# Kernel optimization log

Hardware: AMD Instinct MI355X
Metric: run time of the kernel (lower is better)

The kernel has to match this reference:

```python
import jax, jax.numpy as jnp
import numpy as np

D_MODEL = 768
N_HEADS = 12
D_HEAD = D_MODEL // N_HEADS

def setup_inputs() -> dict:
    key = jax.random.key(0)
    ks = jax.random.split(key, 5)
    B, T = 2, 4096
    x = jax.random.normal(ks[0], (B, T, D_MODEL), dtype=jnp.float32)
    s_in = 1.0 / np.sqrt(D_MODEL)
    W_qkv = jax.random.normal(ks[1], (D_MODEL, 3 * D_MODEL), dtype=jnp.float32) * s_in
    b_qkv = jnp.zeros((3 * D_MODEL,), dtype=jnp.float32)
    W_proj = jax.random.normal(ks[2], (D_MODEL, D_MODEL), dtype=jnp.float32) * s_in
    b_proj = jnp.zeros((D_MODEL,), dtype=jnp.float32)
    return {"x": x, "W_qkv": W_qkv, "b_qkv": b_qkv, "W_proj": W_proj, "b_proj": b_proj}

def reference(x, W_qkv, b_qkv, W_proj, b_proj):
    B, T, C = x.shape
    qkv = x @ W_qkv + b_qkv                      # [B,T,3C]
    q, k, v = jnp.split(qkv, 3, axis=-1)
    def heads(t):
        return t.reshape(B, T, N_HEADS, D_HEAD).transpose(0, 2, 1, 3)  # [B,H,T,d]
    q, k, v = heads(q), heads(k), heads(v)
    scale = 1.0 / np.sqrt(D_HEAD)
    att = jnp.einsum('bhqd,bhkd->bhqk', q, k) * scale  # [B,H,T,T]
    causal = jnp.tril(jnp.ones((T, T), dtype=bool))
    att = jnp.where(causal[None, None], att, -jnp.inf)
    att = jax.nn.softmax(att, axis=-1)
    y = jnp.einsum('bhqk,bhkd->bhqd', att, v)          # [B,H,T,d]
    y = y.transpose(0, 2, 1, 3).reshape(B, T, C)
    return y @ W_proj + b_proj
```

## Files before the change

### kernel.cpp

```cpp
#include <hip/hip_runtime.h>
#include <hip/hip_bf16.h>

typedef __bf16 bf16_t;
typedef bf16_t bf16x4 __attribute__((ext_vector_type(4)));
typedef bf16_t bf16x8 __attribute__((ext_vector_type(8)));
typedef float  f32x4  __attribute__((ext_vector_type(4)));

#define TSEQ   4096
#define NBATCH 2
#define DMODEL 768
#define NHEADS 12
#define DHEAD  64
#define NTOK   (NBATCH*TSEQ)
#define NQKV   (3*DMODEL)

#define QSCALE 0.18033688011112042f
#define SMAX 24.0f

__device__ __forceinline__ f32x4 mfma16(bf16x8 a, bf16x8 b, f32x4 c) {
  return __builtin_amdgcn_mfma_f32_16x16x32_bf16(a, b, c, 0, 0, 0);
}

__device__ __forceinline__ void glds16(const bf16_t* g, bf16_t* l) {
  __builtin_amdgcn_global_load_lds(
      (const __attribute__((address_space(1))) void*)g,
      (__attribute__((address_space(3))) void*)l, 16, 0, 0);
}
__device__ __forceinline__ void glds16f(const float* g, float* l) {
  __builtin_amdgcn_global_load_lds(
      (const __attribute__((address_space(1))) void*)g,
      (__attribute__((address_space(3))) void*)l, 16, 0, 0);
}

__global__ __launch_bounds__(256) void k_transpose_cvt2(
    const float* __restrict__ W1, bf16_t* __restrict__ O1,
    const float* __restrict__ W2, bf16_t* __restrict__ O2) {
  __shared__ bf16_t tile[64][66];
  int t = blockIdx.x;
  const float* in; bf16_t* out; int R, C, c0, r0;
  if (t < 432) { in = W1; out = O1; R = DMODEL; C = NQKV;
                 c0 = (t % 36) * 64; r0 = (t / 36) * 64; }
  else { t -= 432; in = W2; out = O2; R = DMODEL; C = DMODEL;
         c0 = (t % 12) * 64; r0 = (t / 12) * 64; }
  const int tid = threadIdx.x;
  const int r = tid >> 2, cb = (tid & 3) * 16;
  const float* ip = in + (long)(r0 + r) * C + c0 + cb;
#pragma unroll
  for (int k = 0; k < 16; k += 4) {
    float4 v = *(const float4*)(ip + k);
    tile[r][cb + k + 0] = (bf16_t)v.x;
    tile[r][cb + k + 1] = (bf16_t)v.y;
    tile[r][cb + k + 2] = (bf16_t)v.z;
    tile[r][cb + k + 3] = (bf16_t)v.w;
  }
  __syncthreads();
  const int c = tid >> 2, rb = (tid & 3) * 16;
  bf16_t* op = out + (long)(c0 + c) * R + r0 + rb;
  bf16x8 v0, v1;
#pragma unroll
  for (int i = 0; i < 8; ++i) { v0[i] = tile[rb + i][c]; v1[i] = tile[rb + 8 + i][c]; }
  *(bf16x8*)(op) = v0;
  *(bf16x8*)(op + 8) = v1;
}

__global__ __launch_bounds__(256) void k_gemm_qkv(
    const float* __restrict__ X, const bf16_t* __restrict__ Bt,
    const float* __restrict__ bias,
    bf16_t* __restrict__ Qo, bf16_t* __restrict__ Ko, bf16_t* __restrict__ Vt) {
  __shared__ __align__(16) float  Asf[2 * 128 * 32];
  __shared__ __align__(16) bf16_t Bs[2 * 128 * 32];
  const int wave = threadIdx.x >> 6;
  const int lane = threadIdx.x & 63;
  const int quad = lane >> 4;
  const int l16  = lane & 15;
  const int m0 = blockIdx.x * 128;
  const int n0 = blockIdx.y * 128;

  const int arow = lane >> 3;
  const int achk = (lane & 7) ^ arow;
  const float* x0 = X + (long)(m0 + wave * 8 + arow) * DMODEL + achk * 4;
  const int srow = lane >> 2;
  const int scol = (lane & 3) * 8;
  const bf16_t* b0 = Bt + (long)(n0 + wave * 16 + srow) * DMODEL + scol;

  f32x4 acc[2][8] = {};

#pragma unroll
  for (int i = 0; i < 4; ++i)
    glds16f(x0 + (long)i * 32 * DMODEL, Asf + (i * 32 + wave * 8) * 32);
  glds16(b0,               Bs + wave * 16 * 32);
  glds16(b0 + 64 * DMODEL, Bs + (64 + wave * 16) * 32);
  __syncthreads();

  const int sk = l16 & 7;
  for (int ks = 0; ks < DMODEL / 32; ++ks) {
    const int p = ks & 1;
    if (ks + 1 < DMODEL / 32) {
      const int k1 = (ks + 1) * 32;
      float*  Asx = (p ? Asf : Asf + 128 * 32);
      bf16_t* Bsx = (p ? Bs : Bs + 128 * 32);
#pragma unroll
      for (int i = 0; i < 4; ++i)
        glds16f(x0 + (long)i * 32 * DMODEL + k1, Asx + (i * 32 + wave * 8) * 32);
      glds16(b0 + k1,               Bsx + wave * 16 * 32);
      glds16(b0 + 64 * DMODEL + k1, Bsx + (64 + wave * 16) * 32);
    }
    const float*  Ap = Asf + p * (128 * 32);
    const bf16_t* Bp = Bs + p * (128 * 32);

    const int r0 = wave * 32 + l16, r1 = r0 + 16;
    f32x4 a0lo = *(const f32x4*)(Ap + r0 * 32 + (((2 * quad)     ^ sk) << 2));
    f32x4 a0hi = *(const f32x4*)(Ap + r0 * 32 + (((2 * quad + 1) ^ sk) << 2));
    f32x4 a1lo = *(const f32x4*)(Ap + r1 * 32 + (((2 * quad)     ^ sk) << 2));
    f32x4 a1hi = *(const f32x4*)(Ap + r1 * 32 + (((2 * quad + 1) ^ sk) << 2));
    bf16x8 af0, af1;
#pragma unroll
    for (int j = 0; j < 4; ++j) {
      af0[j] = (bf16_t)a0lo[j]; af0[4 + j] = (bf16_t)a0hi[j];
      af1[j] = (bf16_t)a1lo[j]; af1[4 + j] = (bf16_t)a1hi[j];
    }
#pragma unroll
    for (int nt = 0; nt < 8; ++nt) {
      bf16x8 bfm = *(const bf16x8*)(Bp + (nt * 16 + l16) * 32 + quad * 8);
      acc[0][nt] = mfma16(af0, bfm, acc[0][nt]);
      acc[1][nt] = mfma16(af1, bfm, acc[1][nt]);
    }
    __syncthreads();
  }

#pragma unroll
  for (int s = 0; s < 2; ++s)
#pragma unroll
    for (int nt = 0; nt < 8; ++nt) {
      const int n = n0 + nt * 16 + l16;
      const float bv = bias[n];
      const int mb = m0 + wave * 32 + s * 16 + quad * 4;
      const int b = mb >> 12;
      const int t = mb & 4095;
      if (n < DMODEL) {
        const int h = n >> 6, d = n & 63;
        bf16_t* qp = Qo + (((long)(b * NHEADS + h) * TSEQ + t) << 6) + d;
#pragma unroll
        for (int j = 0; j < 4; ++j)
          qp[(long)j << 6] = (bf16_t)((acc[s][nt][j] + bv) * QSCALE);
      } else if (n < 2 * DMODEL) {
        const int n2 = n - DMODEL, h = n2 >> 6, d = n2 & 63;
        bf16_t* kp = Ko + (((long)(b * NHEADS + h) * TSEQ + t) << 6) + d;
#pragma unroll
        for (int j = 0; j < 4; ++j)
          kp[(long)j << 6] = (bf16_t)(acc[s][nt][j] + bv);
      } else {
        const int n2 = n - 2 * DMODEL, h = n2 >> 6, d = n2 & 63;
        bf16x4 v;
#pragma unroll
        for (int j = 0; j < 4; ++j) v[j] = (bf16_t)(acc[s][nt][j] + bv);
        *(bf16x4*)(Vt + ((long)(b * NHEADS + h) * DHEAD + d) * TSEQ + t) = v;
      }
    }
}

__global__ __launch_bounds__(256) void k_gemm_proj(
    const bf16_t* __restrict__ P0, const bf16_t* __restrict__ P1,
    const float* __restrict__ L0, const float* __restrict__ L1,
    const bf16_t* __restrict__ Bt, const float* __restrict__ bias,
    float* __restrict__ out) {
  __shared__ __align__(16) bf16_t A0s[2 * 64 * 32];
  __shared__ __align__(16) bf16_t A1s[2 * 64 * 32];
  __shared__ __align__(16) bf16_t Bs[2 * 128 * 32];
  __shared__ float linv[NHEADS * 64];
  const int wave = threadIdx.x >> 6;
  const int lane = threadIdx.x & 63;
  const int quad = lane >> 4;
  const int l16  = lane & 15;
  const int m0 = blockIdx.x * 64;
  const int n0 = blockIdx.y * 128;
  const int b  = m0 >> 12;
  const int t0 = m0 & 4095;

  for (int i = threadIdx.x; i < NHEADS * 64; i += 256) {
    const int h = i >> 6, t = i & 63;
    const long idx = (long)(b * NHEADS + h) * TSEQ + t0 + t;
    linv[i] = 1.f / (L0[idx] + L1[idx]);
  }

  const int srow = lane >> 2;
  const int scol = (lane & 3) * 8;
  const bf16_t* b0 = Bt + (long)(n0 + wave * 16 + srow) * DMODEL + scol;
  const long arowbase = (long)(t0 + wave * 16 + srow);

  f32x4 acc[8] = {};

  {
    const long off = (((long)(b * NHEADS + 0) * TSEQ + arowbase) << 6) + scol;
    glds16(P0 + off, A0s + wave * 16 * 32);
    glds16(P1 + off, A1s + wave * 16 * 32);
  }
  glds16(b0,               Bs + wave * 16 * 32);
  glds16(b0 + 64 * DMODEL, Bs + (64 + wave * 16) * 32);
  __syncthreads();

  for (int ks = 0; ks < DMODEL / 32; ++ks) {
    const int p = ks & 1;
    if (ks + 1 < DMODEL / 32) {
      const int k1 = (ks + 1) * 32;
      const int ksn = ks + 1;
      bf16_t* A0x = (p ? A0s : A0s + 64 * 32);
      bf16_t* A1x = (p ? A1s : A1s + 64 * 32);
      bf16_t* Bsx = (p ? Bs : Bs + 128 * 32);
      const long off = (((long)(b * NHEADS + (ksn >> 1)) * TSEQ + arowbase) << 6)
                       + ((ksn & 1) << 5) + scol;
      glds16(P0 + off, A0x + wave * 16 * 32);
      glds16(P1 + off, A1x + wave * 16 * 32);
      glds16(b0 + k1,               Bsx + wave * 16 * 32);
      glds16(b0 + 64 * DMODEL + k1, Bsx + (64 + wave * 16) * 32);
    }
    const bf16_t* A0p = A0s + p * (64 * 32);
    const bf16_t* A1p = A1s + p * (64 * 32);
    const bf16_t* Bp  = Bs + p * (128 * 32);

    bf16x8 a0 = *(const bf16x8*)(A0p + (wave * 16 + l16) * 32 + quad * 8);
    bf16x8 a1 = *(const bf16x8*)(A1p + (wave * 16 + l16) * 32 + quad * 8);
    const float li = linv[(ks >> 1) * 64 + wave * 16 + l16];
    bf16x8 af;
#pragma unroll
    for (int j = 0; j < 8; ++j)
      af[j] = (bf16_t)(((float)a0[j] + (float)a1[j]) * li);
#pragma unroll
    for (int nt = 0; nt < 8; ++nt) {
      bf16x8 bfm = *(const bf16x8*)(Bp + (nt * 16 + l16) * 32 + quad * 8);
      acc[nt] = mfma16(af, bfm, acc[nt]);
    }
    __syncthreads();
  }

#pragma unroll
  for (int nt = 0; nt < 8; ++nt) {
    const int n = n0 + nt * 16 + l16;
    const float bv = bias[n];
#pragma unroll
    for (int j = 0; j < 4; ++j) {
      const int m = m0 + wave * 16 + quad * 4 + j;
      out[(long)m * DMODEL + n] = acc[nt][j] + bv;
    }
  }
}

__global__ __launch_bounds__(256, 2) void k_attn(
    const bf16_t* __restrict__ Q, const bf16_t* __restrict__ K,
    const bf16_t* __restrict__ Vt,
    bf16_t* __restrict__ P0, bf16_t* __restrict__ P1,
    float* __restrict__ L0, float* __restrict__ L1) {
  __shared__ __align__(16) bf16_t kbuf[2][64 * 64];
  __shared__ __align__(16) bf16_t vbuf[2][64 * 64];
  const int wave = threadIdx.x >> 6;
  const int lane = threadIdx.x & 63;
  const int quad = lane >> 4;
  const int l16  = lane & 15;
  const int bh = blockIdx.x;
  const int qt = 15 - (blockIdx.y >> 1);
  const int sp = blockIdx.y & 1;
  const int half = 2 * qt + 2;
  const int c0 = sp ? half : 0;
  const int niter = half;
  bf16_t* Pp = sp ? P1 : P0;
  float*  Lp = sp ? L1 : L0;

  const bf16_t* Qh = Q + ((long)bh * TSEQ << 6);
  const bf16_t* Kh = K + ((long)bh * TSEQ << 6);
  const bf16_t* Vh = Vt + (long)bh * DHEAD * TSEQ;

  const int qbase = qt * 256 + wave * 64;

  bf16x8 qf[4][2];
#pragma unroll
  for (int s = 0; s < 4; ++s) {
    const bf16_t* qrow = Qh + ((long)(qbase + s * 16 + l16) << 6);
    qf[s][0] = *(const bf16x8*)(qrow + quad * 8);
    qf[s][1] = *(const bf16x8*)(qrow + 32 + quad * 8);
  }

  f32x4 acc[4][4] = {};
  float lS[4] = {0.f, 0.f, 0.f, 0.f};
  const f32x4 minit = {-SMAX, -SMAX, -SMAX, -SMAX};

  const int kperm = ((l16 >> 2) << 3) + (l16 & 3);
  const int swl = l16 & 7;
  const int srow = lane >> 3;
  const int cV = (lane & 7) ^ (srow & 7);
  const int cK0 = (lane & 7) ^ (srow & 3);
  const int cK1 = cK0 ^ 4;
  const int r0a = wave * 16, r0b = wave * 16 + 8;

  {
    const int k00 = c0 << 6;
    glds16(Kh + ((long)(k00 + r0a + srow) << 6) + cK0 * 8, &kbuf[0][r0a * 64]);
    glds16(Kh + ((long)(k00 + r0b + srow) << 6) + cK1 * 8, &kbuf[0][r0b * 64]);
    glds16(Vh + (long)(r0a + srow) * TSEQ + k00 + cV * 8,  &vbuf[0][r0a * 64]);
    glds16(Vh + (long)(r0b + srow) * TSEQ + k00 + cV * 8,  &vbuf[0][r0b * 64]);
  }
  __syncthreads();

  for (int ci = 0; ci < niter; ++ci) {
    const int p = ci & 1;
    const int k0 = (c0 + ci) << 6;
    if (ci + 1 < niter) {
      const int k1 = k0 + 64;
      glds16(Kh + ((long)(k1 + r0a + srow) << 6) + cK0 * 8, &kbuf[1 - p][r0a * 64]);
      glds16(Kh + ((long)(k1 + r0b + srow) << 6) + cK1 * 8, &kbuf[1 - p][r0b * 64]);
      glds16(Vh + (long)(r0a + srow) * TSEQ + k1 + cV * 8,  &vbuf[1 - p][r0a * 64]);
      glds16(Vh + (long)(r0b + srow) * TSEQ + k1 + cV * 8,  &vbuf[1 - p][r0b * 64]);
    }
    const bf16_t* kb = kbuf[p];
    const bf16_t* vb = vbuf[p];

#pragma unroll
    for (int g = 0; g < 2; ++g) {
      const int rw0 = (g * 32 + kperm) * 64;
      const int rw1 = (g * 32 + 4 + kperm) * 64;
      bf16x8 kf00 = *(const bf16x8*)(kb + rw0 + ((quad ^ swl) << 3));
      bf16x8 kf01 = *(const bf16x8*)(kb + rw0 + (((quad + 4) ^ swl) << 3));
      bf16x8 kf10 = *(const bf16x8*)(kb + rw1 + ((quad ^ swl) << 3));
      bf16x8 kf11 = *(const bf16x8*)(kb + rw1 + (((quad + 4) ^ swl) << 3));
      const bool domask = (k0 + g * 32 + 31 > qbase);

      bf16x8 pf[4];
#pragma unroll
      for (int s = 0; s < 4; ++s) {
        f32x4 st0 = minit, st1 = minit;
        st0 = mfma16(kf00, qf[s][0], st0);
        st0 = mfma16(kf01, qf[s][1], st0);
        st1 = mfma16(kf10, qf[s][0], st1);
        st1 = mfma16(kf11, qf[s][1], st1);
        if (domask) {
          const int qS = qbase + s * 16 + l16;
          const int kb0 = k0 + g * 32 + quad * 8;
#pragma unroll
          for (int j = 0; j < 4; ++j) {
            if (kb0 + j > qS)     st0[j] = -1e30f;
            if (kb0 + 4 + j > qS) st1[j] = -1e30f;
          }
        }
        float rs = 0.f;
#pragma unroll
        for (int j = 0; j < 4; ++j) {
          float e0 = __builtin_amdgcn_exp2f(st0[j]);
          float e1 = __builtin_amdgcn_exp2f(st1[j]);
          rs += e0 + e1;
          pf[s][j]     = (bf16_t)e0;
          pf[s][4 + j] = (bf16_t)e1;
        }
        lS[s] += rs;
      }
#pragma unroll
      for (int dt = 0; dt < 4; ++dt) {
        const int row = dt * 16 + l16;
        bf16x8 vf = *(const bf16x8*)(vb + row * 64 + ((((g << 2) + quad) ^ swl) << 3));
#pragma unroll
        for (int s = 0; s < 4; ++s)
          acc[s][dt] = mfma16(vf, pf[s], acc[s][dt]);
      }
    }
    __syncthreads();
  }

#pragma unroll
  for (int s = 0; s < 4; ++s) {
    lS[s] += __shfl_xor(lS[s], 16);
    lS[s] += __shfl_xor(lS[s], 32);
  }
#pragma unroll
  for (int s = 0; s < 4; ++s) {
    const int qS = qbase + s * 16 + l16;
    bf16_t* prow = Pp + (((long)bh * TSEQ + qS) << 6);
#pragma unroll
    for (int dt = 0; dt < 4; ++dt) {
      bf16x4 w;
#pragma unroll
      for (int j = 0; j < 4; ++j) w[j] = (bf16_t)acc[s][dt][j];
      *(bf16x4*)(prow + dt * 16 + quad * 4) = w;
    }
    if (quad == 0) Lp[(long)bh * TSEQ + qS] = lS[s];
  }
}

extern "C" void kernel_launch(void* const* d_in, const int* in_sizes, int n_in,
                              void* d_out, int out_size, void* d_ws, size_t ws_size,
                              hipStream_t stream) {
  (void)in_sizes; (void)n_in; (void)out_size; (void)ws_size;
  const float* x     = (const float*)d_in[0];
  const float* Wqkv  = (const float*)d_in[1];
  const float* bqkv  = (const float*)d_in[2];
  const float* Wproj = (const float*)d_in[3];
  const float* bproj = (const float*)d_in[4];
  float* out = (float*)d_out;

  char* ws = (char*)d_ws;
  bf16_t* wqkv_t  = (bf16_t*)ws; ws += (long)NQKV * DMODEL * 2;
  bf16_t* wproj_t = (bf16_t*)ws; ws += (long)DMODEL * DMODEL * 2;
  bf16_t* Qb      = (bf16_t*)ws; ws += (long)NTOK * DMODEL * 2;
  bf16_t* Kb      = (bf16_t*)ws; ws += (long)NTOK * DMODEL * 2;
  bf16_t* Vtb     = (bf16_t*)ws; ws += (long)NTOK * DMODEL * 2;
  bf16_t* P0b     = (bf16_t*)ws; ws += (long)NTOK * DMODEL * 2;
  bf16_t* P1b     = (bf16_t*)ws; ws += (long)NTOK * DMODEL * 2;
  float*  L0b     = (float*)ws;  ws += (long)NHEADS * NBATCH * TSEQ * 4;
  float*  L1b     = (float*)ws;  ws += (long)NHEADS * NBATCH * TSEQ * 4;

  k_transpose_cvt2<<<576, 256, 0, stream>>>(Wqkv, wqkv_t, Wproj, wproj_t);
  k_gemm_qkv<<<dim3(NTOK / 128, NQKV / 128), 256, 0, stream>>>(x, wqkv_t, bqkv, Qb, Kb, Vtb);
  k_attn<<<dim3(NBATCH * NHEADS, 32), 256, 0, stream>>>(Qb, Kb, Vtb, P0b, P1b, L0b, L1b);
  k_gemm_proj<<<dim3(NTOK / 64, DMODEL / 128), 256, 0, stream>>>(
      P0b, P1b, L0b, L1b, wproj_t, bproj, out);
}
```

Before: 224.5 us.

## Split attention KV range four ways instead of two

The attention kernel now splits each query tile's causal key range into four chunks instead of two. This doubles the grid to 64 blocks per head-batch. Each chunk writes its own unnormalized partial output and row sum, and the projection GEMM sums all four before normalizing. The aim is more parallelism and better load balance across CUs, at the cost of extra partial-buffer traffic and more loads in the projection GEMM.

```diff
diff --git a/kernel.cpp b/kernel.cpp
--- a/kernel.cpp
+++ b/kernel.cpp
@@ -161,11 +161,15 @@
 
 __global__ __launch_bounds__(256) void k_gemm_proj(
     const bf16_t* __restrict__ P0, const bf16_t* __restrict__ P1,
+    const bf16_t* __restrict__ P2, const bf16_t* __restrict__ P3,
     const float* __restrict__ L0, const float* __restrict__ L1,
+    const float* __restrict__ L2, const float* __restrict__ L3,
     const bf16_t* __restrict__ Bt, const float* __restrict__ bias,
     float* __restrict__ out) {
   __shared__ __align__(16) bf16_t A0s[2 * 64 * 32];
   __shared__ __align__(16) bf16_t A1s[2 * 64 * 32];
+  __shared__ __align__(16) bf16_t A2s[2 * 64 * 32];
+  __shared__ __align__(16) bf16_t A3s[2 * 64 * 32];
   __shared__ __align__(16) bf16_t Bs[2 * 128 * 32];
   __shared__ float linv[NHEADS * 64];
   const int wave = threadIdx.x >> 6;
@@ -180,7 +184,7 @@
   for (int i = threadIdx.x; i < NHEADS * 64; i += 256) {
     const int h = i >> 6, t = i & 63;
     const long idx = (long)(b * NHEADS + h) * TSEQ + t0 + t;
-    linv[i] = 1.f / (L0[idx] + L1[idx]);
+    linv[i] = 1.f / (L0[idx] + L1[idx] + L2[idx] + L3[idx]);
   }
 
   const int srow = lane >> 2;
@@ -194,6 +198,8 @@
     const long off = (((long)(b * NHEADS + 0) * TSEQ + arowbase) << 6) + scol;
     glds16(P0 + off, A0s + wave * 16 * 32);
     glds16(P1 + off, A1s + wave * 16 * 32);
+    glds16(P2 + off, A2s + wave * 16 * 32);
+    glds16(P3 + off, A3s + wave * 16 * 32);
   }
   glds16(b0,               Bs + wave * 16 * 32);
   glds16(b0 + 64 * DMODEL, Bs + (64 + wave * 16) * 32);
@@ -206,25 +212,34 @@
       const int ksn = ks + 1;
       bf16_t* A0x = (p ? A0s : A0s + 64 * 32);
       bf16_t* A1x = (p ? A1s : A1s + 64 * 32);
+      bf16_t* A2x = (p ? A2s : A2s + 64 * 32);
+      bf16_t* A3x = (p ? A3s : A3s + 64 * 32);
       bf16_t* Bsx = (p ? Bs : Bs + 128 * 32);
       const long off = (((long)(b * NHEADS + (ksn >> 1)) * TSEQ + arowbase) << 6)
                        + ((ksn & 1) << 5) + scol;
       glds16(P0 + off, A0x + wave * 16 * 32);
       glds16(P1 + off, A1x + wave * 16 * 32);
+      glds16(P2 + off, A2x + wave * 16 * 32);
+      glds16(P3 + off, A3x + wave * 16 * 32);
       glds16(b0 + k1,               Bsx + wave * 16 * 32);
       glds16(b0 + 64 * DMODEL + k1, Bsx + (64 + wave * 16) * 32);
     }
     const bf16_t* A0p = A0s + p * (64 * 32);
     const bf16_t* A1p = A1s + p * (64 * 32);
+    const bf16_t* A2p = A2s + p * (64 * 32);
+    const bf16_t* A3p = A3s + p * (64 * 32);
     const bf16_t* Bp  = Bs + p * (128 * 32);
 
     bf16x8 a0 = *(const bf16x8*)(A0p + (wave * 16 + l16) * 32 + quad * 8);
     bf16x8 a1 = *(const bf16x8*)(A1p + (wave * 16 + l16) * 32 + quad * 8);
+    bf16x8 a2 = *(const bf16x8*)(A2p + (wave * 16 + l16) * 32 + quad * 8);
+    bf16x8 a3 = *(const bf16x8*)(A3p + (wave * 16 + l16) * 32 + quad * 8);
     const float li = linv[(ks >> 1) * 64 + wave * 16 + l16];
     bf16x8 af;
 #pragma unroll
     for (int j = 0; j < 8; ++j)
-      af[j] = (bf16_t)(((float)a0[j] + (float)a1[j]) * li);
+      af[j] = (bf16_t)((((float)a0[j] + (float)a1[j]) +
+                        ((float)a2[j] + (float)a3[j])) * li);
 #pragma unroll
     for (int nt = 0; nt < 8; ++nt) {
       bf16x8 bfm = *(const bf16x8*)(Bp + (nt * 16 + l16) * 32 + quad * 8);
@@ -249,7 +264,9 @@
     const bf16_t* __restrict__ Q, const bf16_t* __restrict__ K,
     const bf16_t* __restrict__ Vt,
     bf16_t* __restrict__ P0, bf16_t* __restrict__ P1,
-    float* __restrict__ L0, float* __restrict__ L1) {
+    bf16_t* __restrict__ P2, bf16_t* __restrict__ P3,
+    float* __restrict__ L0, float* __restrict__ L1,
+    float* __restrict__ L2, float* __restrict__ L3) {
   __shared__ __align__(16) bf16_t kbuf[2][64 * 64];
   __shared__ __align__(16) bf16_t vbuf[2][64 * 64];
   const int wave = threadIdx.x >> 6;
@@ -257,13 +274,13 @@
   const int quad = lane >> 4;
   const int l16  = lane & 15;
   const int bh = blockIdx.x;
-  const int qt = 15 - (blockIdx.y >> 1);
-  const int sp = blockIdx.y & 1;
-  const int half = 2 * qt + 2;
-  const int c0 = sp ? half : 0;
-  const int niter = half;
-  bf16_t* Pp = sp ? P1 : P0;
-  float*  Lp = sp ? L1 : L0;
+  const int qt = 15 - (blockIdx.y >> 2);
+  const int sp = blockIdx.y & 3;
+  const int quarter = qt + 1;
+  const int c0 = sp * quarter;
+  const int niter = quarter;
+  bf16_t* Pp = (sp == 0) ? P0 : (sp == 1) ? P1 : (sp == 2) ? P2 : P3;
+  float*  Lp = (sp == 0) ? L0 : (sp == 1) ? L1 : (sp == 2) ? L2 : L3;
 
   const bf16_t* Qh = Q + ((long)bh * TSEQ << 6);
   const bf16_t* Kh = K + ((long)bh * TSEQ << 6);
@@ -402,12 +419,17 @@
   bf16_t* Vtb     = (bf16_t*)ws; ws += (long)NTOK * DMODEL * 2;
   bf16_t* P0b     = (bf16_t*)ws; ws += (long)NTOK * DMODEL * 2;
   bf16_t* P1b     = (bf16_t*)ws; ws += (long)NTOK * DMODEL * 2;
+  bf16_t* P2b     = (bf16_t*)ws; ws += (long)NTOK * DMODEL * 2;
+  bf16_t* P3b     = (bf16_t*)ws; ws += (long)NTOK * DMODEL * 2;
   float*  L0b     = (float*)ws;  ws += (long)NHEADS * NBATCH * TSEQ * 4;
   float*  L1b     = (float*)ws;  ws += (long)NHEADS * NBATCH * TSEQ * 4;
+  float*  L2b     = (float*)ws;  ws += (long)NHEADS * NBATCH * TSEQ * 4;
+  float*  L3b     = (float*)ws;  ws += (long)NHEADS * NBATCH * TSEQ * 4;
 
   k_transpose_cvt2<<<576, 256, 0, stream>>>(Wqkv, wqkv_t, Wproj, wproj_t);
   k_gemm_qkv<<<dim3(NTOK / 128, NQKV / 128), 256, 0, stream>>>(x, wqkv_t, bqkv, Qb, Kb, Vtb);
-  k_attn<<<dim3(NBATCH * NHEADS, 32), 256, 0, stream>>>(Qb, Kb, Vtb, P0b, P1b, L0b, L1b);
+  k_attn<<<dim3(NBATCH * NHEADS, 64), 256, 0, stream>>>(
+      Qb, Kb, Vtb, P0b, P1b, P2b, P3b, L0b, L1b, L2b, L3b);
   k_gemm_proj<<<dim3(NTOK / 64, DMODEL / 128), 256, 0, stream>>>(
-      P0b, P1b, L0b, L1b, wproj_t, bproj, out);
-}
+      P0b, P1b, P2b, P3b, L0b, L1b, L2b, L3b, wproj_t, bproj, out);
+}
```

Measured after the change: 236.4 us. +5.3%, slower.

## Deepen attention K/V LDS pipeline to four buffers with two-ahead prefetch

Applied to the files above, without the earlier changes.

Grows the K and V shared-memory ring from two to four buffers and issues global-to-LDS loads two iterations ahead. The full __syncthreads is replaced with an explicit vmcnt wait that leaves the newest chunk in flight, followed by a raw s_barrier. The aim is to hide memory latency better and avoid draining all loads at every step. It doubles LDS use per block to 64KB, which may limit occupancy under the launch bound of two blocks, and leans on hand-written wait counts being correct.

```diff
diff --git a/kernel.cpp b/kernel.cpp
--- a/kernel.cpp
+++ b/kernel.cpp
@@ -250,8 +250,8 @@
     const bf16_t* __restrict__ Vt,
     bf16_t* __restrict__ P0, bf16_t* __restrict__ P1,
     float* __restrict__ L0, float* __restrict__ L1) {
-  __shared__ __align__(16) bf16_t kbuf[2][64 * 64];
-  __shared__ __align__(16) bf16_t vbuf[2][64 * 64];
+  __shared__ __align__(16) bf16_t kbuf[4][64 * 64];
+  __shared__ __align__(16) bf16_t vbuf[4][64 * 64];
   const int wave = threadIdx.x >> 6;
   const int lane = threadIdx.x & 63;
   const int quad = lane >> 4;
@@ -291,25 +291,26 @@
   const int cK1 = cK0 ^ 4;
   const int r0a = wave * 16, r0b = wave * 16 + 8;
 
-  {
-    const int k00 = c0 << 6;
-    glds16(Kh + ((long)(k00 + r0a + srow) << 6) + cK0 * 8, &kbuf[0][r0a * 64]);
-    glds16(Kh + ((long)(k00 + r0b + srow) << 6) + cK1 * 8, &kbuf[0][r0b * 64]);
-    glds16(Vh + (long)(r0a + srow) * TSEQ + k00 + cV * 8,  &vbuf[0][r0a * 64]);
-    glds16(Vh + (long)(r0b + srow) * TSEQ + k00 + cV * 8,  &vbuf[0][r0b * 64]);
-  }
-  __syncthreads();
+  auto issue = [&](int c) {
+    const int kk = (c0 + c) << 6;
+    bf16_t* kd = &kbuf[c & 3][0];
+    bf16_t* vd = &vbuf[c & 3][0];
+    glds16(Kh + ((long)(kk + r0a + srow) << 6) + cK0 * 8, kd + r0a * 64);
+    glds16(Kh + ((long)(kk + r0b + srow) << 6) + cK1 * 8, kd + r0b * 64);
+    glds16(Vh + (long)(r0a + srow) * TSEQ + kk + cV * 8,  vd + r0a * 64);
+    glds16(Vh + (long)(r0b + srow) * TSEQ + kk + cV * 8,  vd + r0b * 64);
+  };
+
+  issue(0);
+  issue(1);
+  asm volatile("s_waitcnt vmcnt(4)" ::: "memory");
+  __builtin_amdgcn_s_barrier();
+  __builtin_amdgcn_sched_barrier(0);
 
   for (int ci = 0; ci < niter; ++ci) {
-    const int p = ci & 1;
+    if (ci + 2 < niter) issue(ci + 2);
+    const int p = ci & 3;
     const int k0 = (c0 + ci) << 6;
-    if (ci + 1 < niter) {
-      const int k1 = k0 + 64;
-      glds16(Kh + ((long)(k1 + r0a + srow) << 6) + cK0 * 8, &kbuf[1 - p][r0a * 64]);
-      glds16(Kh + ((long)(k1 + r0b + srow) << 6) + cK1 * 8, &kbuf[1 - p][r0b * 64]);
-      glds16(Vh + (long)(r0a + srow) * TSEQ + k1 + cV * 8,  &vbuf[1 - p][r0a * 64]);
-      glds16(Vh + (long)(r0b + srow) * TSEQ + k1 + cV * 8,  &vbuf[1 - p][r0b * 64]);
-    }
     const bf16_t* kb = kbuf[p];
     const bf16_t* vb = vbuf[p];
 
@@ -360,7 +361,16 @@
           acc[s][dt] = mfma16(vf, pf[s], acc[s][dt]);
       }
     }
-    __syncthreads();
+
+    if (ci + 1 < niter) {
+      if (ci + 2 < niter) {
+        asm volatile("s_waitcnt vmcnt(4)" ::: "memory");
+      } else {
+        asm volatile("s_waitcnt vmcnt(0)" ::: "memory");
+      }
+      __builtin_amdgcn_s_barrier();
+      __builtin_amdgcn_sched_barrier(0);
+    }
   }
 
 #pragma unroll
```

New measurement: 227.3 us. Within noise of the previous version (+1.3%).
